# Performance work log

Hardware: AMD Instinct MI355X
Metric: run time of the kernel (lower is better)

## Reference

```python
import jax, jax.numpy as jnp
import numpy as np

N = 100000
E = 1600000
IN_FEATS = 512
H1, F1 = 8, 8          # layer1: 8 heads x 8 units
H2, F2 = 1, 40         # layer2: 1 head x out_feats
NEG_SLOPE = 0.2


def setup_inputs() -> dict:
    key = jax.random.key(0)
    ks = jax.random.split(key, 12)
    x = jax.random.normal(ks[0], (N, IN_FEATS), dtype=jnp.float32)
    src = jax.random.randint(ks[1], (E,), 0, N, dtype=jnp.int32)
    dst = jax.random.randint(ks[2], (E,), 0, N, dtype=jnp.int32)
    # Xavier-ish init for params
    W1 = jax.random.normal(ks[3], (IN_FEATS, H1 * F1), dtype=jnp.float32) * (1.0 / np.sqrt(IN_FEATS))
    al1 = jax.random.normal(ks[4], (H1, F1), dtype=jnp.float32) * 0.1
    ar1 = jax.random.normal(ks[5], (H1, F1), dtype=jnp.float32) * 0.1
    b1 = jnp.zeros((H1 * F1,), dtype=jnp.float32)
    W2 = jax.random.normal(ks[6], (H1 * F1, H2 * F2), dtype=jnp.float32) * (1.0 / np.sqrt(H1 * F1))
    al2 = jax.random.normal(ks[7], (H2, F2), dtype=jnp.float32) * 0.1
    ar2 = jax.random.normal(ks[8], (H2, F2), dtype=jnp.float32) * 0.1
    b2 = jnp.zeros((H2 * F2,), dtype=jnp.float32)
    return {"x": x, "src": src, "dst": dst,
            "W1": W1, "al1": al1, "ar1": ar1, "b1": b1,
            "W2": W2, "al2": al2, "ar2": ar2, "b2": b2}


def _gat_conv(feat, src, dst, W, al, ar, b, activation):
    """DGL-style GATConv (dropout disabled / eval mode)."""
    n = feat.shape[0]
    heads, fdim = al.shape
    h = (feat @ W).reshape(n, heads, fdim)            # [N, H, F]
    el = jnp.einsum('nhf,hf->nh', h, al)              # [N, H]
    er = jnp.einsum('nhf,hf->nh', h, ar)              # [N, H]
    e = jax.nn.leaky_relu(el[src] + er[dst], NEG_SLOPE)   # [E, H]
    # edge softmax over incoming edges of each dst node (numerically stable)
    m = jax.ops.segment_max(e, dst, num_segments=n)   # [N, H]
    ex = jnp.exp(e - m[dst])
    s = jax.ops.segment_sum(ex, dst, num_segments=n)  # [N, H]
    alpha = ex / s[dst]                               # [E, H]
    msg = h[src] * alpha[:, :, None]                  # [E, H, F]
    rst = jax.ops.segment_sum(msg, dst, num_segments=n)  # [N, H, F]
    rst = rst + b.reshape(1, heads, fdim)
    if activation is not None:
        rst = activation(rst)
    return rst


def reference(x, src, dst, W1, al1, ar1, b1, W2, al2, ar2, b2):
    h1 = _gat_conv(x, src, dst, W1, al1, ar1, b1, jax.nn.elu)   # [N, H1, F1]
    h1 = h1.reshape(x.shape[0], H1 * F1)                        # flatten(1)
    h2 = _gat_conv(h1, src, dst, W2, al2, ar2, b2, None)        # [N, 1, F2]
    logits = h2.mean(axis=1)                                    # [N, F2]
    return jax.nn.log_softmax(logits, axis=1)
```

## Files before the change

kernel.cpp:

```cpp
#include <hip/hip_runtime.h>
#include <cstdint>
#include <cstddef>

#define IN_F 512
#define C1 64
#define NH 8
#define FD 8
#define C2 40
#define NEG 0.2f

typedef __attribute__((ext_vector_type(8))) short bf16x8;
typedef __attribute__((ext_vector_type(4))) float f32x4;

__device__ inline unsigned short f32_to_bf16_rne(float f) {
    unsigned int u = __float_as_uint(f);
    unsigned int r = (u + 0x7FFFu + ((u >> 16) & 1u)) >> 16;
    return (unsigned short)r;
}
__device__ inline float bf16_to_f32(unsigned short s) {
    return __uint_as_float(((unsigned int)s) << 16);
}

__global__ __launch_bounds__(256) void hist_k(const int* __restrict__ dst, int* __restrict__ deg,
                                              int* __restrict__ pos, int E) {
    int e = blockIdx.x * 256 + threadIdx.x;
    if (e < E) pos[e] = atomicAdd(&deg[dst[e]], 1);
}

__global__ __launch_bounds__(1024) void scan_local_k(const int* __restrict__ deg, int* __restrict__ rowp,
                                                     int* __restrict__ bsums, int n) {
    __shared__ int tmp[1024];
    int tx = threadIdx.x;
    int i = blockIdx.x * 1024 + tx;
    int v = (i < n) ? deg[i] : 0;
    tmp[tx] = v;
    __syncthreads();
    for (int d = 1; d < 1024; d <<= 1) {
        int t = (tx >= d) ? tmp[tx - d] : 0;
        __syncthreads();
        tmp[tx] += t;
        __syncthreads();
    }
    if (i < n) rowp[i] = tmp[tx] - v;
    if (tx == 1023) bsums[blockIdx.x] = tmp[tx];
}

__global__ __launch_bounds__(128) void scan_sums_k(int* bsums, int nb) {
    __shared__ int tmp[128];
    int tx = threadIdx.x;
    int v = (tx < nb) ? bsums[tx] : 0;
    tmp[tx] = v;
    __syncthreads();
    for (int d = 1; d < 128; d <<= 1) {
        int t = (tx >= d) ? tmp[tx - d] : 0;
        __syncthreads();
        tmp[tx] += t;
        __syncthreads();
    }
    if (tx < nb) bsums[tx] = tmp[tx] - v;
}

__global__ __launch_bounds__(1024) void scan_add_k(int* rowp, const int* __restrict__ bsums, int n) {
    int i = blockIdx.x * 1024 + threadIdx.x;
    if (i < n) rowp[i] += bsums[blockIdx.x];
}

__global__ __launch_bounds__(256) void scatter_k(const int* __restrict__ src, const int* __restrict__ dst,
                                                 const int* __restrict__ rowp, const int* __restrict__ pos,
                                                 int* __restrict__ csr_src, int E) {
    int e = blockIdx.x * 256 + threadIdx.x;
    if (e >= E) return;
    csr_src[rowp[dst[e]] + pos[e]] = src[e];
}

__global__ __launch_bounds__(256) void wt_pre_k(const float* __restrict__ W1,
                                                unsigned short* __restrict__ wt_hi,
                                                unsigned short* __restrict__ wt_lo) {
    int id = blockIdx.x * 256 + threadIdx.x;
    if (id >= IN_F * C1) return;
    int col = id & (C1 - 1);
    int k = id >> 6;
    float w = W1[id];
    unsigned short hb = f32_to_bf16_rne(w);
    unsigned short lb = f32_to_bf16_rne(w - bf16_to_f32(hb));
    wt_hi[(size_t)col * IN_F + k] = hb;
    wt_lo[(size_t)col * IN_F + k] = lb;
}

__global__ __launch_bounds__(256) void gemm1_mfma_k(const float* __restrict__ x,
                                                    const unsigned short* __restrict__ wt_hi,
                                                    const unsigned short* __restrict__ wt_lo,
                                                    const float* __restrict__ al, const float* __restrict__ ar,
                                                    unsigned short* __restrict__ hb_out,
                                                    float* __restrict__ el, float* __restrict__ er, int N) {
    __shared__ alignas(16) unsigned short wlds[2][8192];
    const int tid = threadIdx.x;
    const int wave = tid >> 6, lane = tid & 63;
    const int m = lane & 15, q = lane >> 4;
    const int row = blockIdx.x * 64 + wave * 16 + m;
    const int row_c = row < N ? row : N - 1;
    const float* xp = x + (size_t)row_c * IN_F + q * 8;

    f32x4 acc[4];
#pragma unroll
    for (int ct = 0; ct < 4; ct++) acc[ct] = (f32x4){0.f, 0.f, 0.f, 0.f};
    float4 xr[2][4];

#define WLOAD(c, buf)                                                                              \
    {                                                                                              \
        _Pragma("unroll") for (int j_ = 0; j_ < 4; j_++) {                                         \
            int slot_ = j_ * 256 + wave * 64 + lane;                                               \
            const unsigned short* gbase_ = (slot_ < 512) ? wt_hi : wt_lo;                          \
            int s_ = slot_ & 511;                                                                  \
            int col_ = s_ & 63, kq_ = s_ >> 6;                                                     \
            const unsigned short* g_ = gbase_ + (size_t)col_ * IN_F + (c) * 64 + kq_ * 8;          \
            unsigned short* l_ = &wlds[buf][0] + (size_t)(j_ * 256 + wave * 64) * 8;               \
            __builtin_amdgcn_global_load_lds((const __attribute__((address_space(1))) unsigned int*)g_, \
                                             (__attribute__((address_space(3))) unsigned int*)l_,  \
                                             16, 0, 0);                                            \
        }                                                                                          \
    }
#define XLOAD(c, r)                                  \
    {                                                \
        const float* xsrc_ = xp + (c) * 64;          \
        (r)[0] = *(const float4*)(xsrc_);            \
        (r)[1] = *(const float4*)(xsrc_ + 4);        \
        (r)[2] = *(const float4*)(xsrc_ + 32);       \
        (r)[3] = *(const float4*)(xsrc_ + 36);       \
    }

    WLOAD(0, 0);
    XLOAD(0, xr[0]);

    for (int c = 0; c < 8; c++) {
        int p = c & 1;
        __syncthreads();
        if (c < 7) {
            WLOAD(c + 1, p ^ 1);
            XLOAD(c + 1, xr[p ^ 1]);
        }
#pragma unroll
        for (int ki = 0; ki < 2; ki++) {
            float f[8];
            f[0] = xr[p][ki * 2].x; f[1] = xr[p][ki * 2].y; f[2] = xr[p][ki * 2].z; f[3] = xr[p][ki * 2].w;
            f[4] = xr[p][ki * 2 + 1].x; f[5] = xr[p][ki * 2 + 1].y; f[6] = xr[p][ki * 2 + 1].z; f[7] = xr[p][ki * 2 + 1].w;
            unsigned int u[8], lu[8];
#pragma unroll
            for (int j = 0; j < 8; j++) u[j] = __float_as_uint(f[j]);
            union { uint4 u4; bf16x8 v; } H, L;
            H.u4.x = __builtin_amdgcn_perm(u[1], u[0], 0x07060302u);
            H.u4.y = __builtin_amdgcn_perm(u[3], u[2], 0x07060302u);
            H.u4.z = __builtin_amdgcn_perm(u[5], u[4], 0x07060302u);
            H.u4.w = __builtin_amdgcn_perm(u[7], u[6], 0x07060302u);
#pragma unroll
            for (int j = 0; j < 8; j++)
                lu[j] = __float_as_uint(f[j] - __uint_as_float(u[j] & 0xFFFF0000u));
            L.u4.x = __builtin_amdgcn_perm(lu[1], lu[0], 0x07060302u);
            L.u4.y = __builtin_amdgcn_perm(lu[3], lu[2], 0x07060302u);
            L.u4.z = __builtin_amdgcn_perm(lu[5], lu[4], 0x07060302u);
            L.u4.w = __builtin_amdgcn_perm(lu[7], lu[6], 0x07060302u);
            int kq = ki * 4 + q;
#pragma unroll
            for (int ct = 0; ct < 4; ct++) {
                int slot = kq * 64 + ct * 16 + m;
                bf16x8 bh = *(const bf16x8*)&wlds[p][slot * 8];
                bf16x8 bl = *(const bf16x8*)&wlds[p][4096 + slot * 8];
                acc[ct] = __builtin_amdgcn_mfma_f32_16x16x32_bf16(H.v, bh, acc[ct], 0, 0, 0);
                acc[ct] = __builtin_amdgcn_mfma_f32_16x16x32_bf16(L.v, bh, acc[ct], 0, 0, 0);
                acc[ct] = __builtin_amdgcn_mfma_f32_16x16x32_bf16(H.v, bl, acc[ct], 0, 0, 0);
            }
        }
    }
    int rbase = blockIdx.x * 64 + wave * 16 + q * 4;
#pragma unroll
    for (int r = 0; r < 4; r++) {
        int ro = rbase + r;
        if (ro < N) {
#pragma unroll
            for (int ct = 0; ct < 4; ct++)
                hb_out[(size_t)ro * C1 + ct * 16 + m] = f32_to_bf16_rne(acc[ct][r]);
        }
    }

    __syncthreads();
    float* hst = (float*)&wlds[0][0];
    {
        int rr = wave * 16 + q * 4;
#pragma unroll
        for (int r = 0; r < 4; r++)
#pragma unroll
            for (int ct = 0; ct < 4; ct++)
                hst[(rr + r) * 69 + ct * 16 + m] = acc[ct][r];
    }
    __syncthreads();
    for (int id = tid; id < 512; id += 256) {
        int r = id >> 3, hd = id & 7;
        int nn = blockIdx.x * 64 + r;
        if (nn < N) {
            float e_l = 0.f, e_r = 0.f;
#pragma unroll
            for (int f = 0; f < 8; f++) {
                float v = hst[r * 69 + hd * 8 + f];
                e_l += v * al[hd * 8 + f];
                e_r += v * ar[hd * 8 + f];
            }
            el[(size_t)nn * NH + hd] = e_l;
            er[(size_t)nn * NH + hd] = e_r;
        }
    }
#undef WLOAD
#undef XLOAD
}

__global__ __launch_bounds__(256) void l1_wave_k(const unsigned short* __restrict__ hb,
                                                 const float* __restrict__ el, const float* __restrict__ er,
                                                 const int* __restrict__ rowp, const int* __restrict__ deg,
                                                 const int* __restrict__ csr_src, const float* __restrict__ b1,
                                                 float* __restrict__ h1out, int N) {
    int n = (blockIdx.x * 256 + threadIdx.x) >> 6;
    if (n >= N) return;
    int lane = threadIdx.x & 63;
    int half = lane >> 5;
    int fl = lane & 31;
    int hg = fl >> 2;
    int start = rowp[n], cnt = deg[n];
    float erd = er[(size_t)n * NH + hg];
    const unsigned int* hb32 = (const unsigned int*)hb;
    const int* cp = csr_src + start;
    float acc0 = 0.f, acc1 = 0.f, s = 0.f;
    int i = 0;
    for (; i + 8 <= cnt; i += 8) {
        int sA = cp[i + half];
        int sB = cp[i + 2 + half];
        int sC = cp[i + 4 + half];
        int sD = cp[i + 6 + half];
        float eA = el[(size_t)sA * NH + hg];
        float eB = el[(size_t)sB * NH + hg];
        float eC = el[(size_t)sC * NH + hg];
        float eD = el[(size_t)sD * NH + hg];
        unsigned int qA = hb32[(size_t)sA * 32 + fl];
        unsigned int qB = hb32[(size_t)sB * 32 + fl];
        unsigned int qC = hb32[(size_t)sC * 32 + fl];
        unsigned int qD = hb32[(size_t)sD * 32 + fl];
        eA += erd; eB += erd; eC += erd; eD += erd;
        eA = eA > 0.f ? eA : NEG * eA;
        eB = eB > 0.f ? eB : NEG * eB;
        eC = eC > 0.f ? eC : NEG * eC;
        eD = eD > 0.f ? eD : NEG * eD;
        float wA = __expf(eA), wB = __expf(eB), wC = __expf(eC), wD = __expf(eD);
        s += (wA + wB) + (wC + wD);
        acc0 += wA * __uint_as_float(qA << 16) + wB * __uint_as_float(qB << 16) +
                wC * __uint_as_float(qC << 16) + wD * __uint_as_float(qD << 16);
        acc1 += wA * __uint_as_float(qA & 0xFFFF0000u) + wB * __uint_as_float(qB & 0xFFFF0000u) +
                wC * __uint_as_float(qC & 0xFFFF0000u) + wD * __uint_as_float(qD & 0xFFFF0000u);
    }
    for (; i + 2 <= cnt; i += 2) {
        int sn = cp[i + half];
        float e = el[(size_t)sn * NH + hg] + erd;
        e = e > 0.f ? e : NEG * e;
        float w = __expf(e);
        unsigned int qv = hb32[(size_t)sn * 32 + fl];
        s += w;
        acc0 += w * __uint_as_float(qv << 16);
        acc1 += w * __uint_as_float(qv & 0xFFFF0000u);
    }
    if (i < cnt && half == 0) {
        int sn = cp[i];
        float e = el[(size_t)sn * NH + hg] + erd;
        e = e > 0.f ? e : NEG * e;
        float w = __expf(e);
        unsigned int qv = hb32[(size_t)sn * 32 + fl];
        s += w;
        acc0 += w * __uint_as_float(qv << 16);
        acc1 += w * __uint_as_float(qv & 0xFFFF0000u);
    }
    acc0 += __shfl_xor(acc0, 32);
    acc1 += __shfl_xor(acc1, 32);
    s += __shfl_xor(s, 32);
    float sinv = (s > 0.f) ? 1.f / s : 0.f;
    float2 bv = *(const float2*)(b1 + fl * 2);
    float o0 = acc0 * sinv + bv.x;
    float o1 = acc1 * sinv + bv.y;
    o0 = o0 > 0.f ? o0 : (__expf(o0) - 1.f);
    o1 = o1 > 0.f ? o1 : (__expf(o1) - 1.f);
    if (half == 0) *(float2*)(h1out + (size_t)n * C1 + fl * 2) = make_float2(o0, o1);
}

__global__ __launch_bounds__(256) void gemm2_attn2_k(const float* __restrict__ h1, const float* __restrict__ W2,
                                                     const float* __restrict__ al2, const float* __restrict__ ar2,
                                                     unsigned short* __restrict__ h2b, float* __restrict__ el2,
                                                     float* __restrict__ er2, int N) {
    __shared__ float ws[C1 * C2];
    __shared__ float hs[64][C1];
    __shared__ float h2s[64][C2];
    __shared__ float a2s[2 * C2];
    int t = threadIdx.x;
    int n0 = blockIdx.x * 64;
    for (int i = t; i < C1 * C2; i += 256) ws[i] = W2[i];
    if (t < C2) a2s[t] = al2[t];
    else if (t < 2 * C2) a2s[t] = ar2[t - C2];
    for (int i = t; i < 64 * 16; i += 256) {
        int r = i >> 4, c4 = i & 15;
        int n = n0 + r;
        float4 v = (n < N) ? *(const float4*)(h1 + (size_t)n * C1 + c4 * 4) : make_float4(0.f, 0.f, 0.f, 0.f);
        *(float4*)&hs[r][c4 * 4] = v;
    }
    __syncthreads();
    for (int o = t; o < 64 * C2; o += 256) {
        int r = o / C2, c = o % C2;
        float sum = 0.f;
#pragma unroll
        for (int k = 0; k < C1; k++) sum += hs[r][k] * ws[k * C2 + c];
        h2s[r][c] = sum;
    }
    __syncthreads();
    unsigned int* h2d = (unsigned int*)h2b;
    for (int o = t; o < 64 * 20; o += 256) {
        int r = o / 20, cd = o % 20;
        int nn = n0 + r;
        if (nn < N) {
            unsigned int lo16 = f32_to_bf16_rne(h2s[r][cd * 2]);
            unsigned int hi16 = f32_to_bf16_rne(h2s[r][cd * 2 + 1]);
            h2d[(size_t)nn * 20 + cd] = lo16 | (hi16 << 16);
        }
    }
    if (t < 64) {
        int nn = n0 + t;
        if (nn < N) {
            float e_l = 0.f, e_r = 0.f;
#pragma unroll
            for (int c = 0; c < C2; c++) {
                float v = h2s[t][c];
                e_l += v * a2s[c];
                e_r += v * a2s[C2 + c];
            }
            el2[nn] = e_l;
            er2[nn] = e_r;
        }
    }
}

__global__ __launch_bounds__(256) void l2_fused_k(const unsigned short* __restrict__ h2b,
                                                  const float* __restrict__ el, const float* __restrict__ er,
                                                  const int* __restrict__ rowp, const int* __restrict__ deg,
                                                  const int* __restrict__ csr_src, const float* __restrict__ b2,
                                                  float* __restrict__ out, int N) {
    int tid = threadIdx.x;
    int n = blockIdx.x * 32 + (tid >> 3);
    int sub = tid & 7;
    if (n >= N) return;
    float vals[8];
    if (sub < 5) {
        int start = rowp[n], cnt = deg[n];
        float erd = er[n];
        float s = 0.f;
        float acc[8];
#pragma unroll
        for (int j = 0; j < 8; j++) acc[j] = 0.f;
        const int* cp = csr_src + start;
        int i = 0;
        for (; i + 4 <= cnt; i += 4) {
            int sn0 = cp[i], sn1 = cp[i + 1], sn2 = cp[i + 2], sn3 = cp[i + 3];
            float e0 = el[sn0], e1 = el[sn1], e2 = el[sn2], e3 = el[sn3];
            bf16x8 v0 = *(const bf16x8*)(h2b + (size_t)sn0 * C2 + sub * 8);
            bf16x8 v1 = *(const bf16x8*)(h2b + (size_t)sn1 * C2 + sub * 8);
            bf16x8 v2 = *(const bf16x8*)(h2b + (size_t)sn2 * C2 + sub * 8);
            bf16x8 v3 = *(const bf16x8*)(h2b + (size_t)sn3 * C2 + sub * 8);
            e0 += erd; e1 += erd; e2 += erd; e3 += erd;
            e0 = e0 > 0.f ? e0 : NEG * e0;
            e1 = e1 > 0.f ? e1 : NEG * e1;
            e2 = e2 > 0.f ? e2 : NEG * e2;
            e3 = e3 > 0.f ? e3 : NEG * e3;
            float w0 = __expf(e0), w1 = __expf(e1), w2 = __expf(e2), w3 = __expf(e3);
            s += (w0 + w1) + (w2 + w3);
#pragma unroll
            for (int j = 0; j < 8; j++) {
                acc[j] += w0 * bf16_to_f32((unsigned short)v0[j]) + w1 * bf16_to_f32((unsigned short)v1[j]) +
                          w2 * bf16_to_f32((unsigned short)v2[j]) + w3 * bf16_to_f32((unsigned short)v3[j]);
            }
        }
        for (; i < cnt; i++) {
            int sn = cp[i];
            float e = el[sn] + erd;
            e = e > 0.f ? e : NEG * e;
            float w0 = __expf(e);
            s += w0;
            bf16x8 v = *(const bf16x8*)(h2b + (size_t)sn * C2 + sub * 8);
#pragma unroll
            for (int j = 0; j < 8; j++) acc[j] += w0 * bf16_to_f32((unsigned short)v[j]);
        }
        float sinv = (s > 0.f) ? 1.f / s : 0.f;
        const float* bp = b2 + sub * 8;
#pragma unroll
        for (int j = 0; j < 8; j++) vals[j] = acc[j] * sinv + bp[j];
    } else {
#pragma unroll
        for (int j = 0; j < 8; j++) vals[j] = -1e30f;
    }
    float mx = vals[0];
#pragma unroll
    for (int j = 1; j < 8; j++) mx = fmaxf(mx, vals[j]);
#pragma unroll
    for (int off = 1; off < 8; off <<= 1) mx = fmaxf(mx, __shfl_xor(mx, off, 8));
    float se = 0.f;
#pragma unroll
    for (int j = 0; j < 8; j++) se += __expf(vals[j] - mx);
#pragma unroll
    for (int off = 1; off < 8; off <<= 1) se += __shfl_xor(se, off, 8);
    float ls = __logf(se) + mx;
    if (sub < 5) {
        float* op = out + (size_t)n * C2 + sub * 8;
        *(float4*)(op) = make_float4(vals[0] - ls, vals[1] - ls, vals[2] - ls, vals[3] - ls);
        *(float4*)(op + 4) = make_float4(vals[4] - ls, vals[5] - ls, vals[6] - ls, vals[7] - ls);
    }
}

extern "C" void kernel_launch(void* const* d_in, const int* in_sizes, int n_in,
                              void* d_out, int out_size, void* d_ws, size_t ws_size,
                              hipStream_t stream) {
    (void)n_in; (void)out_size; (void)ws_size;
    const float* x   = (const float*)d_in[0];
    const int*   src = (const int*)d_in[1];
    const int*   dst = (const int*)d_in[2];
    const float* W1  = (const float*)d_in[3];
    const float* al1 = (const float*)d_in[4];
    const float* ar1 = (const float*)d_in[5];
    const float* b1  = (const float*)d_in[6];
    const float* W2  = (const float*)d_in[7];
    const float* al2 = (const float*)d_in[8];
    const float* ar2 = (const float*)d_in[9];
    const float* b2  = (const float*)d_in[10];
    float* out = (float*)d_out;
    const int N = in_sizes[0] / IN_F;
    const int E = in_sizes[1];

    char* w = (char*)d_ws;
    auto alloc = [&](size_t bytes) -> char* {
        char* p = w;
        w += (bytes + 255) & ~(size_t)255;
        return p;
    };
    int* deg     = (int*)alloc((size_t)N * 4);
    int* rowp    = (int*)alloc((size_t)N * 4);
    int* bsums   = (int*)alloc(512);
    int* pos     = (int*)alloc((size_t)E * 4);
    int* csr_src = (int*)alloc((size_t)E * 4);
    unsigned short* wt_hi = (unsigned short*)alloc((size_t)IN_F * C1 * 2);
    unsigned short* wt_lo = (unsigned short*)alloc((size_t)IN_F * C1 * 2);
    unsigned short* hb    = (unsigned short*)alloc((size_t)N * C1 * 2);
    float* el1   = (float*)alloc((size_t)N * NH * 4);
    float* er1   = (float*)alloc((size_t)N * NH * 4);
    float* h1    = (float*)alloc((size_t)N * C1 * 4);
    unsigned short* h2b = (unsigned short*)alloc((size_t)N * C2 * 2);
    float* el2   = (float*)alloc((size_t)N * 4);
    float* er2   = (float*)alloc((size_t)N * 4);

    hipMemsetAsync(deg, 0, (size_t)N * 4, stream);

    int ebl = (E + 255) / 256;
    int nb = (N + 1023) / 1024;
    hist_k<<<ebl, 256, 0, stream>>>(dst, deg, pos, E);
    scan_local_k<<<nb, 1024, 0, stream>>>(deg, rowp, bsums, N);
    scan_sums_k<<<1, 128, 0, stream>>>(bsums, nb);
    scan_add_k<<<nb, 1024, 0, stream>>>(rowp, bsums, N);
    scatter_k<<<ebl, 256, 0, stream>>>(src, dst, rowp, pos, csr_src, E);

    wt_pre_k<<<(IN_F * C1 + 255) / 256, 256, 0, stream>>>(W1, wt_hi, wt_lo);
    gemm1_mfma_k<<<(N + 63) / 64, 256, 0, stream>>>(x, wt_hi, wt_lo, al1, ar1, hb, el1, er1, N);
    l1_wave_k<<<(N * 64 + 255) / 256, 256, 0, stream>>>(hb, el1, er1, rowp, deg, csr_src, b1, h1, N);
    gemm2_attn2_k<<<(N + 63) / 64, 256, 0, stream>>>(h1, W2, al2, ar2, h2b, el2, er2, N);
    l2_fused_k<<<(N + 31) / 32, 256, 0, stream>>>(h2b, el2, er2, rowp, deg, csr_src, b2, out, N);
}
```

Before: 598.2 us.

## Use split-bf16 MFMA for layer-2 GEMM, fuse scan kernels, prefetch CSR indices

Layer 2's scalar FP32 GEMM from shared memory is replaced by bf16 MFMA with hi/lo split precision, using W2 pretransposed in the combined weight-prep kernel. The block-sum scan kernel is folded into the add kernel, with each block reducing the preceding block sums itself. The layer-1 aggregation now has four lane groups each handling two edges with 64-bit loads, and both aggregation loops software-prefetch the next neighbour indices using masked tails. The aim is fewer launches, cheaper GEMM2 and better latency hiding in the gathers. The cost is extra masked tail work and added shuffle reductions.

```diff
diff --git a/kernel.cpp b/kernel.cpp
--- a/kernel.cpp
+++ b/kernel.cpp
@@ -45,24 +45,28 @@
     if (tx == 1023) bsums[blockIdx.x] = tmp[tx];
 }
 
-__global__ __launch_bounds__(128) void scan_sums_k(int* bsums, int nb) {
-    __shared__ int tmp[128];
+__global__ __launch_bounds__(1024) void scan_add_k(int* rowp, const int* __restrict__ bsums, int n, int nb) {
+    __shared__ int red[128];
     int tx = threadIdx.x;
-    int v = (tx < nb) ? bsums[tx] : 0;
-    tmp[tx] = v;
-    __syncthreads();
-    for (int d = 1; d < 128; d <<= 1) {
-        int t = (tx >= d) ? tmp[tx - d] : 0;
-        __syncthreads();
-        tmp[tx] += t;
-        __syncthreads();
-    }
-    if (tx < nb) bsums[tx] = tmp[tx] - v;
-}
-
-__global__ __launch_bounds__(1024) void scan_add_k(int* rowp, const int* __restrict__ bsums, int n) {
-    int i = blockIdx.x * 1024 + threadIdx.x;
-    if (i < n) rowp[i] += bsums[blockIdx.x];
+    if (tx < 128) red[tx] = (tx < blockIdx.x && tx < nb) ? bsums[tx] : 0;
+    __syncthreads();
+    if (tx < 64) red[tx] += red[tx + 64];
+    __syncthreads();
+    if (tx < 32) red[tx] += red[tx + 32];
+    __syncthreads();
+    if (tx < 16) red[tx] += red[tx + 16];
+    __syncthreads();
+    if (tx < 8) red[tx] += red[tx + 8];
+    __syncthreads();
+    if (tx < 4) red[tx] += red[tx + 4];
+    __syncthreads();
+    if (tx < 2) red[tx] += red[tx + 2];
+    __syncthreads();
+    if (tx == 0) red[0] += red[1];
+    __syncthreads();
+    int off = red[0];
+    int i = blockIdx.x * 1024 + tx;
+    if (i < n) rowp[i] += off;
 }
 
 __global__ __launch_bounds__(256) void scatter_k(const int* __restrict__ src, const int* __restrict__ dst,
@@ -73,18 +77,29 @@
     csr_src[rowp[dst[e]] + pos[e]] = src[e];
 }
 
-__global__ __launch_bounds__(256) void wt_pre_k(const float* __restrict__ W1,
-                                                unsigned short* __restrict__ wt_hi,
-                                                unsigned short* __restrict__ wt_lo) {
+__global__ __launch_bounds__(256) void pre_k(const float* __restrict__ W1, const float* __restrict__ W2,
+                                             unsigned short* __restrict__ wt_hi, unsigned short* __restrict__ wt_lo,
+                                             unsigned short* __restrict__ w2t_hi, unsigned short* __restrict__ w2t_lo) {
     int id = blockIdx.x * 256 + threadIdx.x;
-    if (id >= IN_F * C1) return;
-    int col = id & (C1 - 1);
-    int k = id >> 6;
-    float w = W1[id];
-    unsigned short hb = f32_to_bf16_rne(w);
-    unsigned short lb = f32_to_bf16_rne(w - bf16_to_f32(hb));
-    wt_hi[(size_t)col * IN_F + k] = hb;
-    wt_lo[(size_t)col * IN_F + k] = lb;
+    if (id < IN_F * C1) {
+        int col = id & (C1 - 1);
+        int k = id >> 6;
+        float w = W1[id];
+        unsigned short hb = f32_to_bf16_rne(w);
+        unsigned short lb = f32_to_bf16_rne(w - bf16_to_f32(hb));
+        wt_hi[(size_t)col * IN_F + k] = hb;
+        wt_lo[(size_t)col * IN_F + k] = lb;
+    } else {
+        int id2 = id - IN_F * C1;
+        if (id2 < 48 * 64) {
+            int c = id2 >> 6, k = id2 & 63;
+            float w = (c < C2) ? W2[(size_t)k * C2 + c] : 0.f;
+            unsigned short hb = f32_to_bf16_rne(w);
+            unsigned short lb = f32_to_bf16_rne(w - bf16_to_f32(hb));
+            w2t_hi[c * 64 + k] = hb;
+            w2t_lo[c * 64 + k] = lb;
+        }
+    }
 }
 
 __global__ __launch_bounds__(256) void gemm1_mfma_k(const float* __restrict__ x,
@@ -220,99 +235,130 @@
     int n = (blockIdx.x * 256 + threadIdx.x) >> 6;
     if (n >= N) return;
     int lane = threadIdx.x & 63;
-    int half = lane >> 5;
-    int fl = lane & 31;
-    int hg = fl >> 2;
+    int q = lane >> 4;
+    int f = lane & 15;
+    int hd = f >> 1;
     int start = rowp[n], cnt = deg[n];
-    float erd = er[(size_t)n * NH + hg];
-    const unsigned int* hb32 = (const unsigned int*)hb;
+    float erd = er[(size_t)n * NH + hd];
+    const uint2* hb64 = (const uint2*)hb;
     const int* cp = csr_src + start;
-    float acc0 = 0.f, acc1 = 0.f, s = 0.f;
-    int i = 0;
-    for (; i + 8 <= cnt; i += 8) {
-        int sA = cp[i + half];
-        int sB = cp[i + 2 + half];
-        int sC = cp[i + 4 + half];
-        int sD = cp[i + 6 + half];
-        float eA = el[(size_t)sA * NH + hg];
-        float eB = el[(size_t)sB * NH + hg];
-        float eC = el[(size_t)sC * NH + hg];
-        float eD = el[(size_t)sD * NH + hg];
-        unsigned int qA = hb32[(size_t)sA * 32 + fl];
-        unsigned int qB = hb32[(size_t)sB * 32 + fl];
-        unsigned int qC = hb32[(size_t)sC * 32 + fl];
-        unsigned int qD = hb32[(size_t)sD * 32 + fl];
-        eA += erd; eB += erd; eC += erd; eD += erd;
-        eA = eA > 0.f ? eA : NEG * eA;
-        eB = eB > 0.f ? eB : NEG * eB;
-        eC = eC > 0.f ? eC : NEG * eC;
-        eD = eD > 0.f ? eD : NEG * eD;
-        float wA = __expf(eA), wB = __expf(eB), wC = __expf(eC), wD = __expf(eD);
-        s += (wA + wB) + (wC + wD);
-        acc0 += wA * __uint_as_float(qA << 16) + wB * __uint_as_float(qB << 16) +
-                wC * __uint_as_float(qC << 16) + wD * __uint_as_float(qD << 16);
-        acc1 += wA * __uint_as_float(qA & 0xFFFF0000u) + wB * __uint_as_float(qB & 0xFFFF0000u) +
-                wC * __uint_as_float(qC & 0xFFFF0000u) + wD * __uint_as_float(qD & 0xFFFF0000u);
-    }
-    for (; i + 2 <= cnt; i += 2) {
-        int sn = cp[i + half];
-        float e = el[(size_t)sn * NH + hg] + erd;
-        e = e > 0.f ? e : NEG * e;
-        float w = __expf(e);
-        unsigned int qv = hb32[(size_t)sn * 32 + fl];
-        s += w;
-        acc0 += w * __uint_as_float(qv << 16);
-        acc1 += w * __uint_as_float(qv & 0xFFFF0000u);
-    }
-    if (i < cnt && half == 0) {
-        int sn = cp[i];
-        float e = el[(size_t)sn * NH + hg] + erd;
-        e = e > 0.f ? e : NEG * e;
-        float w = __expf(e);
-        unsigned int qv = hb32[(size_t)sn * 32 + fl];
-        s += w;
-        acc0 += w * __uint_as_float(qv << 16);
-        acc1 += w * __uint_as_float(qv & 0xFFFF0000u);
-    }
-    acc0 += __shfl_xor(acc0, 32);
-    acc1 += __shfl_xor(acc1, 32);
-    s += __shfl_xor(s, 32);
+    float a0 = 0.f, a1 = 0.f, a2 = 0.f, a3 = 0.f, s = 0.f;
+    if (cnt > 0) {
+        int lastc = cnt - 1;
+        int c0 = cp[(q < cnt) ? q : lastc];
+        int c1 = cp[(4 + q < cnt) ? 4 + q : lastc];
+        int i = 0;
+        while (i + 8 < cnt) {
+            int i8 = i + 8;
+            int c2 = cp[(i8 + q < cnt) ? i8 + q : lastc];
+            int c3 = cp[(i8 + 4 + q < cnt) ? i8 + 4 + q : lastc];
+            float e0 = el[(size_t)c0 * NH + hd] + erd;
+            float e1 = el[(size_t)c1 * NH + hd] + erd;
+            uint2 v0 = hb64[(size_t)c0 * 16 + f];
+            uint2 v1 = hb64[(size_t)c1 * 16 + f];
+            e0 = e0 > 0.f ? e0 : NEG * e0;
+            e1 = e1 > 0.f ? e1 : NEG * e1;
+            float w0 = __expf(e0), w1 = __expf(e1);
+            s += w0 + w1;
+            a0 += w0 * __uint_as_float(v0.x << 16) + w1 * __uint_as_float(v1.x << 16);
+            a1 += w0 * __uint_as_float(v0.x & 0xFFFF0000u) + w1 * __uint_as_float(v1.x & 0xFFFF0000u);
+            a2 += w0 * __uint_as_float(v0.y << 16) + w1 * __uint_as_float(v1.y << 16);
+            a3 += w0 * __uint_as_float(v0.y & 0xFFFF0000u) + w1 * __uint_as_float(v1.y & 0xFFFF0000u);
+            c0 = c2; c1 = c3; i = i8;
+        }
+        {
+            bool m0 = (i + q) < cnt, m1 = (i + 4 + q) < cnt;
+            float e0 = el[(size_t)c0 * NH + hd] + erd;
+            float e1 = el[(size_t)c1 * NH + hd] + erd;
+            uint2 v0 = hb64[(size_t)c0 * 16 + f];
+            uint2 v1 = hb64[(size_t)c1 * 16 + f];
+            e0 = e0 > 0.f ? e0 : NEG * e0;
+            e1 = e1 > 0.f ? e1 : NEG * e1;
+            float w0 = m0 ? __expf(e0) : 0.f;
+            float w1 = m1 ? __expf(e1) : 0.f;
+            s += w0 + w1;
+            a0 += w0 * __uint_as_float(v0.x << 16) + w1 * __uint_as_float(v1.x << 16);
+            a1 += w0 * __uint_as_float(v0.x & 0xFFFF0000u) + w1 * __uint_as_float(v1.x & 0xFFFF0000u);
+            a2 += w0 * __uint_as_float(v0.y << 16) + w1 * __uint_as_float(v1.y << 16);
+            a3 += w0 * __uint_as_float(v0.y & 0xFFFF0000u) + w1 * __uint_as_float(v1.y & 0xFFFF0000u);
+        }
+    }
+    a0 += __shfl_xor(a0, 16); a0 += __shfl_xor(a0, 32);
+    a1 += __shfl_xor(a1, 16); a1 += __shfl_xor(a1, 32);
+    a2 += __shfl_xor(a2, 16); a2 += __shfl_xor(a2, 32);
+    a3 += __shfl_xor(a3, 16); a3 += __shfl_xor(a3, 32);
+    s  += __shfl_xor(s, 16);  s  += __shfl_xor(s, 32);
     float sinv = (s > 0.f) ? 1.f / s : 0.f;
-    float2 bv = *(const float2*)(b1 + fl * 2);
-    float o0 = acc0 * sinv + bv.x;
-    float o1 = acc1 * sinv + bv.y;
+    float4 bv = *(const float4*)(b1 + f * 4);
+    float o0 = a0 * sinv + bv.x;
+    float o1 = a1 * sinv + bv.y;
+    float o2 = a2 * sinv + bv.z;
+    float o3 = a3 * sinv + bv.w;
     o0 = o0 > 0.f ? o0 : (__expf(o0) - 1.f);
     o1 = o1 > 0.f ? o1 : (__expf(o1) - 1.f);
-    if (half == 0) *(float2*)(h1out + (size_t)n * C1 + fl * 2) = make_float2(o0, o1);
-}
-
-__global__ __launch_bounds__(256) void gemm2_attn2_k(const float* __restrict__ h1, const float* __restrict__ W2,
+    o2 = o2 > 0.f ? o2 : (__expf(o2) - 1.f);
+    o3 = o3 > 0.f ? o3 : (__expf(o3) - 1.f);
+    if (q == 0) *(float4*)(h1out + (size_t)n * C1 + f * 4) = make_float4(o0, o1, o2, o3);
+}
+
+__global__ __launch_bounds__(256) void gemm2_attn2_k(const float* __restrict__ h1,
+                                                     const unsigned short* __restrict__ w2t_hi,
+                                                     const unsigned short* __restrict__ w2t_lo,
                                                      const float* __restrict__ al2, const float* __restrict__ ar2,
                                                      unsigned short* __restrict__ h2b, float* __restrict__ el2,
                                                      float* __restrict__ er2, int N) {
-    __shared__ float ws[C1 * C2];
-    __shared__ float hs[64][C1];
-    __shared__ float h2s[64][C2];
+    __shared__ float h2s[64][49];
     __shared__ float a2s[2 * C2];
     int t = threadIdx.x;
+    int wave = t >> 6, lane = t & 63;
+    int m = lane & 15, q = lane >> 4;
     int n0 = blockIdx.x * 64;
-    for (int i = t; i < C1 * C2; i += 256) ws[i] = W2[i];
     if (t < C2) a2s[t] = al2[t];
     else if (t < 2 * C2) a2s[t] = ar2[t - C2];
-    for (int i = t; i < 64 * 16; i += 256) {
-        int r = i >> 4, c4 = i & 15;
-        int n = n0 + r;
-        float4 v = (n < N) ? *(const float4*)(h1 + (size_t)n * C1 + c4 * 4) : make_float4(0.f, 0.f, 0.f, 0.f);
-        *(float4*)&hs[r][c4 * 4] = v;
-    }
-    __syncthreads();
-    for (int o = t; o < 64 * C2; o += 256) {
-        int r = o / C2, c = o % C2;
-        float sum = 0.f;
-#pragma unroll
-        for (int k = 0; k < C1; k++) sum += hs[r][k] * ws[k * C2 + c];
-        h2s[r][c] = sum;
-    }
+    int row = n0 + wave * 16 + m;
+    int row_c = row < N ? row : N - 1;
+    const float* hp = h1 + (size_t)row_c * C1 + q * 8;
+    f32x4 acc[3];
+#pragma unroll
+    for (int ct = 0; ct < 3; ct++) acc[ct] = (f32x4){0.f, 0.f, 0.f, 0.f};
+#pragma unroll
+    for (int ks = 0; ks < 2; ks++) {
+        float4 r0 = *(const float4*)(hp + ks * 32);
+        float4 r1 = *(const float4*)(hp + ks * 32 + 4);
+        float f[8];
+        f[0] = r0.x; f[1] = r0.y; f[2] = r0.z; f[3] = r0.w;
+        f[4] = r1.x; f[5] = r1.y; f[6] = r1.z; f[7] = r1.w;
+        unsigned int u[8], lu[8];
+#pragma unroll
+        for (int j = 0; j < 8; j++) u[j] = __float_as_uint(f[j]);
+        union { uint4 u4; bf16x8 v; } H, L;
+        H.u4.x = __builtin_amdgcn_perm(u[1], u[0], 0x07060302u);
+        H.u4.y = __builtin_amdgcn_perm(u[3], u[2], 0x07060302u);
+        H.u4.z = __builtin_amdgcn_perm(u[5], u[4], 0x07060302u);
+        H.u4.w = __builtin_amdgcn_perm(u[7], u[6], 0x07060302u);
+#pragma unroll
+        for (int j = 0; j < 8; j++)
+            lu[j] = __float_as_uint(f[j] - __uint_as_float(u[j] & 0xFFFF0000u));
+        L.u4.x = __builtin_amdgcn_perm(lu[1], lu[0], 0x07060302u);
+        L.u4.y = __builtin_amdgcn_perm(lu[3], lu[2], 0x07060302u);
+        L.u4.z = __builtin_amdgcn_perm(lu[5], lu[4], 0x07060302u);
+        L.u4.w = __builtin_amdgcn_perm(lu[7], lu[6], 0x07060302u);
+        int kb = ks * 32 + q * 8;
+#pragma unroll
+        for (int ct = 0; ct < 3; ct++) {
+            int col = ct * 16 + m;
+            bf16x8 bh = *(const bf16x8*)(w2t_hi + col * 64 + kb);
+            bf16x8 bl = *(const bf16x8*)(w2t_lo + col * 64 + kb);
+            acc[ct] = __builtin_amdgcn_mfma_f32_16x16x32_bf16(H.v, bh, acc[ct], 0, 0, 0);
+            acc[ct] = __builtin_amdgcn_mfma_f32_16x16x32_bf16(L.v, bh, acc[ct], 0, 0, 0);
+            acc[ct] = __builtin_amdgcn_mfma_f32_16x16x32_bf16(H.v, bl, acc[ct], 0, 0, 0);
+        }
+    }
+    int rl = wave * 16 + q * 4;
+#pragma unroll
+    for (int ct = 0; ct < 3; ct++)
+#pragma unroll
+        for (int r = 0; r < 4; r++) h2s[rl + r][ct * 16 + m] = acc[ct][r];
     __syncthreads();
     unsigned int* h2d = (unsigned int*)h2b;
     for (int o = t; o < 64 * 20; o += 256) {
@@ -358,36 +404,61 @@
 #pragma unroll
         for (int j = 0; j < 8; j++) acc[j] = 0.f;
         const int* cp = csr_src + start;
-        int i = 0;
-        for (; i + 4 <= cnt; i += 4) {
-            int sn0 = cp[i], sn1 = cp[i + 1], sn2 = cp[i + 2], sn3 = cp[i + 3];
-            float e0 = el[sn0], e1 = el[sn1], e2 = el[sn2], e3 = el[sn3];
-            bf16x8 v0 = *(const bf16x8*)(h2b + (size_t)sn0 * C2 + sub * 8);
-            bf16x8 v1 = *(const bf16x8*)(h2b + (size_t)sn1 * C2 + sub * 8);
-            bf16x8 v2 = *(const bf16x8*)(h2b + (size_t)sn2 * C2 + sub * 8);
-            bf16x8 v3 = *(const bf16x8*)(h2b + (size_t)sn3 * C2 + sub * 8);
-            e0 += erd; e1 += erd; e2 += erd; e3 += erd;
-            e0 = e0 > 0.f ? e0 : NEG * e0;
-            e1 = e1 > 0.f ? e1 : NEG * e1;
-            e2 = e2 > 0.f ? e2 : NEG * e2;
-            e3 = e3 > 0.f ? e3 : NEG * e3;
-            float w0 = __expf(e0), w1 = __expf(e1), w2 = __expf(e2), w3 = __expf(e3);
-            s += (w0 + w1) + (w2 + w3);
-#pragma unroll
-            for (int j = 0; j < 8; j++) {
-                acc[j] += w0 * bf16_to_f32((unsigned short)v0[j]) + w1 * bf16_to_f32((unsigned short)v1[j]) +
-                          w2 * bf16_to_f32((unsigned short)v2[j]) + w3 * bf16_to_f32((unsigned short)v3[j]);
+        if (cnt > 0) {
+            int last = cnt - 1;
+            int c0 = cp[0];
+            int c1 = cp[1 < cnt ? 1 : last];
+            int c2 = cp[2 < cnt ? 2 : last];
+            int c3 = cp[3 < cnt ? 3 : last];
+            int i = 0;
+            while (i + 4 < cnt) {
+                int i4 = i + 4;
+                int p0 = cp[i4];
+                int p1 = cp[(i4 + 1 < cnt) ? i4 + 1 : last];
+                int p2 = cp[(i4 + 2 < cnt) ? i4 + 2 : last];
+                int p3 = cp[(i4 + 3 < cnt) ? i4 + 3 : last];
+                float e0 = el[c0], e1 = el[c1], e2 = el[c2], e3 = el[c3];
+                bf16x8 v0 = *(const bf16x8*)(h2b + (size_t)c0 * C2 + sub * 8);
+                bf16x8 v1 = *(const bf16x8*)(h2b + (size_t)c1 * C2 + sub * 8);
+                bf16x8 v2 = *(const bf16x8*)(h2b + (size_t)c2 * C2 + sub * 8);
+                bf16x8 v3 = *(const bf16x8*)(h2b + (size_t)c3 * C2 + sub * 8);
+                e0 += erd; e1 += erd; e2 += erd; e3 += erd;
+                e0 = e0 > 0.f ? e0 : NEG * e0;
+                e1 = e1 > 0.f ? e1 : NEG * e1;
+                e2 = e2 > 0.f ? e2 : NEG * e2;
+                e3 = e3 > 0.f ? e3 : NEG * e3;
+                float w0 = __expf(e0), w1 = __expf(e1), w2 = __expf(e2), w3 = __expf(e3);
+                s += (w0 + w1) + (w2 + w3);
+#pragma unroll
+                for (int j = 0; j < 8; j++) {
+                    acc[j] += w0 * bf16_to_f32((unsigned short)v0[j]) + w1 * bf16_to_f32((unsigned short)v1[j]) +
+                              w2 * bf16_to_f32((unsigned short)v2[j]) + w3 * bf16_to_f32((unsigned short)v3[j]);
+                }
+                c0 = p0; c1 = p1; c2 = p2; c3 = p3; i = i4;
             }
-        }
-        for (; i < cnt; i++) {
-            int sn = cp[i];
-            float e = el[sn] + erd;
-            e = e > 0.f ? e : NEG * e;
-            float w0 = __expf(e);
-            s += w0;
-            bf16x8 v = *(const bf16x8*)(h2b + (size_t)sn * C2 + sub * 8);
-#pragma unroll
-            for (int j = 0; j < 8; j++) acc[j] += w0 * bf16_to_f32((unsigned short)v[j]);
+            {
+                bool m0 = i < cnt, m1 = i + 1 < cnt, m2 = i + 2 < cnt, m3 = i + 3 < cnt;
+                float e0 = el[c0], e1 = el[c1], e2 = el[c2], e3 = el[c3];
+                bf16x8 v0 = *(const bf16x8*)(h2b + (size_t)c0 * C2 + sub * 8);
+                bf16x8 v1 = *(const bf16x8*)(h2b + (size_t)c1 * C2 + sub * 8);
+                bf16x8 v2 = *(const bf16x8*)(h2b + (size_t)c2 * C2 + sub * 8);
+                bf16x8 v3 = *(const bf16x8*)(h2b + (size_t)c3 * C2 + sub * 8);
+                e0 += erd; e1 += erd; e2 += erd; e3 += erd;
+                e0 = e0 > 0.f ? e0 : NEG * e0;
+                e1 = e1 > 0.f ? e1 : NEG * e1;
+                e2 = e2 > 0.f ? e2 : NEG * e2;
+                e3 = e3 > 0.f ? e3 : NEG * e3;
+                float w0 = m0 ? __expf(e0) : 0.f;
+                float w1 = m1 ? __expf(e1) : 0.f;
+                float w2 = m2 ? __expf(e2) : 0.f;
+                float w3 = m3 ? __expf(e3) : 0.f;
+                s += (w0 + w1) + (w2 + w3);
+#pragma unroll
+                for (int j = 0; j < 8; j++) {
+                    acc[j] += w0 * bf16_to_f32((unsigned short)v0[j]) + w1 * bf16_to_f32((unsigned short)v1[j]) +
+                              w2 * bf16_to_f32((unsigned short)v2[j]) + w3 * bf16_to_f32((unsigned short)v3[j]);
+                }
+            }
         }
         float sinv = (s > 0.f) ? 1.f / s : 0.f;
         const float* bp = b2 + sub * 8;
@@ -447,6 +518,8 @@
     int* csr_src = (int*)alloc((size_t)E * 4);
     unsigned short* wt_hi = (unsigned short*)alloc((size_t)IN_F * C1 * 2);
     unsigned short* wt_lo = (unsigned short*)alloc((size_t)IN_F * C1 * 2);
+    unsigned short* w2t_hi = (unsigned short*)alloc((size_t)48 * 64 * 2);
+    unsigned short* w2t_lo = (unsigned short*)alloc((size_t)48 * 64 * 2);
     unsigned short* hb    = (unsigned short*)alloc((size_t)N * C1 * 2);
     float* el1   = (float*)alloc((size_t)N * NH * 4);
     float* er1   = (float*)alloc((size_t)N * NH * 4);
@@ -461,13 +534,12 @@
     int nb = (N + 1023) / 1024;
     hist_k<<<ebl, 256, 0, stream>>>(dst, deg, pos, E);
     scan_local_k<<<nb, 1024, 0, stream>>>(deg, rowp, bsums, N);
-    scan_sums_k<<<1, 128, 0, stream>>>(bsums, nb);
-    scan_add_k<<<nb, 1024, 0, stream>>>(rowp, bsums, N);
+    scan_add_k<<<nb, 1024, 0, stream>>>(rowp, bsums, N, nb);
     scatter_k<<<ebl, 256, 0, stream>>>(src, dst, rowp, pos, csr_src, E);
 
-    wt_pre_k<<<(IN_F * C1 + 255) / 256, 256, 0, stream>>>(W1, wt_hi, wt_lo);
+    pre_k<<<(IN_F * C1 + 48 * 64 + 255) / 256, 256, 0, stream>>>(W1, W2, wt_hi, wt_lo, w2t_hi, w2t_lo);
     gemm1_mfma_k<<<(N + 63) / 64, 256, 0, stream>>>(x, wt_hi, wt_lo, al1, ar1, hb, el1, er1, N);
     l1_wave_k<<<(N * 64 + 255) / 256, 256, 0, stream>>>(hb, el1, er1, rowp, deg, csr_src, b1, h1, N);
-    gemm2_attn2_k<<<(N + 63) / 64, 256, 0, stream>>>(h1, W2, al2, ar2, h2b, el2, er2, N);
+    gemm2_attn2_k<<<(N + 63) / 64, 256, 0, stream>>>(h1, w2t_hi, w2t_lo, al2, ar2, h2b, el2, er2, N);
     l2_fused_k<<<(N + 31) / 32, 256, 0, stream>>>(h2b, el2, er2, rowp, deg, csr_src, b2, out, N);
 }
```

Measured after the change: 551.7 us. 7.8% less time.
